# Kernel tuning notes

Measured on AMD Instinct MI355X. Metric: run time of the kernel, lower is better.

Reference implementation:

```python
import jax, jax.numpy as jnp
import numpy as np

LN_EPS = 1e-5


def layer_norm(x, g, b):
    m = jnp.mean(x, axis=-1, keepdims=True)
    v = jnp.mean((x - m) ** 2, axis=-1, keepdims=True)
    return (x - m) * jax.lax.rsqrt(v + LN_EPS) * g + b


def sppcf(x):
    # x: [B, de], de = 4*d. Multi-scale avg-pool + strided interleave assembly.
    B, de = x.shape
    d = de // 4
    p2 = x.reshape(B, de // 2, 2).mean(-1)          # kernel=2, stride=2 -> [B, 2d]
    p4 = x.reshape(B, d, 4).mean(-1)                # kernel=4, stride=4 -> [B, d]
    # kernel=16, stride=4 pooling via cumsum: out[i] = mean(x[:, 4i:4i+16]), i in [0, d-4]
    cs = jnp.concatenate([jnp.zeros((B, 1), x.dtype), jnp.cumsum(x, axis=1)], axis=1)
    starts = jnp.arange(d - 3) * 4
    p16 = (cs[:, starts + 16] - cs[:, starts]) / 16.0  # [B, d-3]
    # fused_output2[:, :-3] = p16 ; fused_output2[:, -3:] = fused_output2[:, -7:-4] = p16[:, -4:-1]
    f2 = jnp.concatenate([p16, p16[:, -4:-1]], axis=1)  # [B, d]
    # out[0::2]=p2, out[1::4]=p4, out[3::4]=f2  <=>  interleave groups of 4
    out = jnp.stack([p2[:, 0::2], p4, p2[:, 1::2], f2], axis=-1).reshape(B, de)
    return out


def setup_inputs() -> dict:
    key = jax.random.key(0)
    ks = jax.random.split(key, 8)
    B, S, C = 16384, 25, 200
    E, D, H, NC = 2, 4 * C, 32, 16  # encoder_n, dim, mlp_dim, num_classes
    inp = {
        "x": jax.random.normal(ks[0], (B, S, C), dtype=jnp.float32),
        "lnA_g": jnp.ones((E, D), jnp.float32),
        "lnA_b": jnp.zeros((E, D), jnp.float32),
        "lnB_g": jnp.ones((E, D), jnp.float32),
        "lnB_b": jnp.zeros((E, D), jnp.float32),
        "w1": jax.random.normal(ks[1], (E, D, H), jnp.float32) * (1.0 / np.sqrt(D)),
        "b1": jnp.zeros((E, H), jnp.float32),
        "w2": jax.random.normal(ks[2], (E, H, D), jnp.float32) * (1.0 / np.sqrt(H)),
        "b2": jnp.zeros((E, D), jnp.float32),
        "fc_w": jax.random.normal(ks[3], (C, NC), jnp.float32) * (1.0 / np.sqrt(C)),
        "fc_b": jnp.zeros((NC,), jnp.float32),
    }
    return inp


def reference(x, lnA_g, lnA_b, lnB_g, lnB_b, w1, b1, w2, b2, fc_w, fc_b):
    B, S, C = x.shape
    E = lnA_g.shape[0]
    # CFModule.cross_fuse: interleave min/mean/last/max over spectral-neighbor axis
    body = x[:, :-1, :]
    h = jnp.stack(
        [body.min(axis=1), body.mean(axis=1), x[:, -1, :], body.max(axis=1)], axis=-1
    ).reshape(B, 4 * C)
    for i in range(E):
        # Residual(PreNorm(SPPCFModule))
        h = h + sppcf(layer_norm(h, lnA_g[i], lnA_b[i]))
        # Residual(PreNorm(FeedForward))  (dropout=0 -> identity)
        z = layer_norm(h, lnB_g[i], lnB_b[i])
        z = jax.nn.gelu(z @ w1[i] + b1[i], approximate=False) @ w2[i] + b2[i]
        h = h + z
    # n_pool=1, channels % 1 == 0 branch: view [B, C, 4].mean then fc0
    pooled = h.reshape(B, C, 4).mean(axis=-1)
    return pooled @ fc_w + fc_b
```

## Files before the change

### kernel.cpp

```cpp
#include <hip/hip_runtime.h>
#include <math.h>

namespace {

constexpr int kC  = 200;
constexpr int kD  = 800;
constexpr int kS  = 25;
constexpr int kH  = 32;
constexpr int kNC = 16;
constexpr int kR  = 8;
constexpr int kRW = 800;

typedef float vfloat4 __attribute__((ext_vector_type(4)));

__device__ __forceinline__ int woff(int m) { return (m << 2) ^ ((m & 0x38) >> 1); }

__device__ __forceinline__ float4 ld4(const float* p) { return *(const float4*)p; }
__device__ __forceinline__ float4 ld4nt(const float* p) {
    vfloat4 v = __builtin_nontemporal_load((const vfloat4*)p);
    return make_float4(v.x, v.y, v.z, v.w);
}
__device__ __forceinline__ void   st4(float* p, float4 v) { *(float4*)p = v; }
__device__ __forceinline__ float  hsum4(float4 v) { return (v.x + v.y) + (v.z + v.w); }

__device__ __forceinline__ float4 f4fma(float s, float4 w, float4 a) {
    a.x = fmaf(s, w.x, a.x); a.y = fmaf(s, w.y, a.y);
    a.z = fmaf(s, w.z, a.z); a.w = fmaf(s, w.w, a.w);
    return a;
}

__device__ __forceinline__ void wfence() {
    asm volatile("s_waitcnt lgkmcnt(0)" ::: "memory");
}

__global__ __launch_bounds__(256)
void featurize_kernel(const float* __restrict__ x, float* __restrict__ hws, int Btot)
{
    const int gid = blockIdx.x * 256 + threadIdx.x;
    if (gid >= Btot * 50) return;
    const int row = gid / 50;
    const int cq  = gid - row * 50;

    const float* xp = x + (size_t)row * (kS * kC) + cq * 4;
    float4 v = ld4nt(xp);
    float4 mn = v, mx = v, sm = v;
    #pragma unroll
    for (int s = 1; s < kS - 1; ++s) {
        float4 u = ld4nt(xp + s * kC);
        mn.x = fminf(mn.x, u.x); mx.x = fmaxf(mx.x, u.x); sm.x += u.x;
        mn.y = fminf(mn.y, u.y); mx.y = fmaxf(mx.y, u.y); sm.y += u.y;
        mn.z = fminf(mn.z, u.z); mx.z = fmaxf(mx.z, u.z); sm.z += u.z;
        mn.w = fminf(mn.w, u.w); mx.w = fmaxf(mx.w, u.w); sm.w += u.w;
    }
    float4 last = ld4nt(xp + (kS - 1) * kC);
    const float i24 = 1.0f / 24.0f;
    float* hp = hws + (size_t)row * kD + 16 * cq;
    st4(hp + 0,  make_float4(mn.x, sm.x * i24, last.x, mx.x));
    st4(hp + 4,  make_float4(mn.y, sm.y * i24, last.y, mx.y));
    st4(hp + 8,  make_float4(mn.z, sm.z * i24, last.z, mx.z));
    st4(hp + 12, make_float4(mn.w, sm.w * i24, last.w, mx.w));
}

__device__ __forceinline__ void ln_row(const float* hrow, float* yrow,
                                       const float* __restrict__ g,
                                       const float* __restrict__ bb, int j)
{
    const bool tail = (j < 8);
    float4 v0 = ld4(&hrow[woff(j)]);
    float4 v1 = ld4(&hrow[woff(j + 64)]);
    float4 v2 = ld4(&hrow[woff(j + 128)]);
    float4 v3 = make_float4(0.f, 0.f, 0.f, 0.f);
    if (tail) v3 = ld4(&hrow[woff(192 + j)]);

    float sm = hsum4(v0) + hsum4(v1) + hsum4(v2) + hsum4(v3);
    #pragma unroll
    for (int mk = 32; mk >= 1; mk >>= 1) sm += __shfl_xor(sm, mk, 64);
    const float mean = sm * (1.0f / 800.0f);

    float ssq = 0.f;
    { float a=v0.x-mean,b=v0.y-mean,c=v0.z-mean,d=v0.w-mean; ssq += a*a+b*b+c*c+d*d; }
    { float a=v1.x-mean,b=v1.y-mean,c=v1.z-mean,d=v1.w-mean; ssq += a*a+b*b+c*c+d*d; }
    { float a=v2.x-mean,b=v2.y-mean,c=v2.z-mean,d=v2.w-mean; ssq += a*a+b*b+c*c+d*d; }
    if (tail) { float a=v3.x-mean,b=v3.y-mean,c=v3.z-mean,d=v3.w-mean; ssq += a*a+b*b+c*c+d*d; }
    #pragma unroll
    for (int mk = 32; mk >= 1; mk >>= 1) ssq += __shfl_xor(ssq, mk, 64);
    const float rstd = rsqrtf(ssq * (1.0f / 800.0f) + 1e-5f);

    auto stc = [&](int m, float4 v) {
        float4 g4 = ld4(&g[4 * m]);
        float4 b4 = ld4(&bb[4 * m]);
        float4 y;
        y.x = (v.x - mean) * rstd * g4.x + b4.x;
        y.y = (v.y - mean) * rstd * g4.y + b4.y;
        y.z = (v.z - mean) * rstd * g4.z + b4.z;
        y.w = (v.w - mean) * rstd * g4.w + b4.w;
        st4(&yrow[woff(m)], y);
    };
    stc(j, v0); stc(j + 64, v1); stc(j + 128, v2);
    if (tail) stc(192 + j, v3);
}

__device__ __forceinline__ void sppcf_add(const float* yrow, float* hrow, int j)
{
    auto one = [&](int m) {
        const int kk = (m <= 196) ? m : m - 4;
        float4 q0 = ld4(&yrow[woff(kk)]);
        float4 q1 = ld4(&yrow[woff(kk + 1)]);
        float4 q2 = ld4(&yrow[woff(kk + 2)]);
        float4 q3 = ld4(&yrow[woff(kk + 3)]);
        float4 y4 = (m <= 196) ? q0 : ld4(&yrow[woff(m)]);
        const float s16 = hsum4(q0) + hsum4(q1) + hsum4(q2) + hsum4(q3);
        float4 h4 = ld4(&hrow[woff(m)]);
        h4.x += (y4.x + y4.y) * 0.5f;
        h4.y += (y4.x + y4.y + y4.z + y4.w) * 0.25f;
        h4.z += (y4.z + y4.w) * 0.5f;
        h4.w += s16 * (1.0f / 16.0f);
        st4(&hrow[woff(m)], h4);
    };
    one(j); one(j + 64); one(j + 128);
    if (j < 8) one(192 + j);
}

template<bool FROMWS>
__global__ __launch_bounds__(256)
void essp_main(const float* __restrict__ src,
               const float* __restrict__ lnA_g, const float* __restrict__ lnA_b,
               const float* __restrict__ lnB_g, const float* __restrict__ lnB_b,
               const float* __restrict__ w1, const float* __restrict__ b1,
               const float* __restrict__ w2, const float* __restrict__ b2,
               const float* __restrict__ fc_w, const float* __restrict__ fc_b,
               float* __restrict__ out, int Btot)
{
    __shared__ float hs[kR * kRW];
    __shared__ float zb[kR * kRW];
    __shared__ float vb[kR * kH];

    const int t   = threadIdx.x;
    const int w   = t >> 6;
    const int j   = t & 63;
    const int b0  = blockIdx.x * kR;

    #pragma unroll
    for (int rr = 0; rr < 2; ++rr) {
        const int lr  = w + 4 * rr;
        const int row = b0 + lr;
        if constexpr (FROMWS) {
            if (row < Btot) {
                const float* hg = src + (size_t)row * kD;
                float* hr = &hs[lr * kRW];
                st4(&hr[woff(j)],       ld4(&hg[4 * j]));
                st4(&hr[woff(j + 64)],  ld4(&hg[4 * (j + 64)]));
                st4(&hr[woff(j + 128)], ld4(&hg[4 * (j + 128)]));
                if (j < 8) st4(&hr[woff(192 + j)], ld4(&hg[4 * (192 + j)]));
            }
        } else {
            if (j < 50 && row < Btot) {
                const float* xp = src + (size_t)row * (kS * kC) + j * 4;
                float4 v = ld4nt(xp);
                float4 mn = v, mx = v, sm = v;
                #pragma unroll
                for (int s = 1; s < kS - 1; ++s) {
                    float4 u = ld4nt(xp + s * kC);
                    mn.x = fminf(mn.x, u.x); mx.x = fmaxf(mx.x, u.x); sm.x += u.x;
                    mn.y = fminf(mn.y, u.y); mx.y = fmaxf(mx.y, u.y); sm.y += u.y;
                    mn.z = fminf(mn.z, u.z); mx.z = fmaxf(mx.z, u.z); sm.z += u.z;
                    mn.w = fminf(mn.w, u.w); mx.w = fmaxf(mx.w, u.w); sm.w += u.w;
                }
                float4 last = ld4nt(xp + (kS - 1) * kC);
                const float i24 = 1.0f / 24.0f;
                float* hr = &hs[lr * kRW];
                st4(&hr[woff(4 * j + 0)], make_float4(mn.x, sm.x * i24, last.x, mx.x));
                st4(&hr[woff(4 * j + 1)], make_float4(mn.y, sm.y * i24, last.y, mx.y));
                st4(&hr[woff(4 * j + 2)], make_float4(mn.z, sm.z * i24, last.z, mx.z));
                st4(&hr[woff(4 * j + 3)], make_float4(mn.w, sm.w * i24, last.w, mx.w));
            }
        }
    }
    wfence();

    for (int layer = 0; layer < 2; ++layer) {
        const float* gA  = lnA_g + layer * kD;
        const float* bAv = lnA_b + layer * kD;
        const float* gB  = lnB_g + layer * kD;
        const float* bBv = lnB_b + layer * kD;
        const float* w1p = w1 + layer * kD * kH;
        const float* b1p = b1 + layer * kH;
        const float* w2p = w2 + layer * kH * kD;
        const float* b2p = b2 + layer * kD;

        ln_row(&hs[w * kRW], &zb[w * kRW], gA, bAv, j);
        ln_row(&hs[(w + 4) * kRW], &zb[(w + 4) * kRW], gA, bAv, j);
        wfence();
        sppcf_add(&zb[w * kRW], &hs[w * kRW], j);
        sppcf_add(&zb[(w + 4) * kRW], &hs[(w + 4) * kRW], j);
        wfence();
        ln_row(&hs[w * kRW], &zb[w * kRW], gB, bBv, j);
        ln_row(&hs[(w + 4) * kRW], &zb[(w + 4) * kRW], gB, bBv, j);
        __syncthreads();

        float4 acc[kR];
        const int dg = t >> 3, cg = t & 7;
        #pragma unroll
        for (int r = 0; r < kR; ++r) acc[r] = make_float4(0.f, 0.f, 0.f, 0.f);
        if (t < 200) {
            #pragma unroll
            for (int cc = 0; cc < 8; ++cc) {
                const int m = dg * 8 + cc, d0 = 4 * m;
                float4 wr0 = ld4(&w1p[(d0 + 0) * kH + 4 * cg]);
                float4 wr1 = ld4(&w1p[(d0 + 1) * kH + 4 * cg]);
                float4 wr2 = ld4(&w1p[(d0 + 2) * kH + 4 * cg]);
                float4 wr3 = ld4(&w1p[(d0 + 3) * kH + 4 * cg]);
                const int wo = woff(m);
                #pragma unroll
                for (int r = 0; r < kR; ++r) {
                    float4 z = ld4(&zb[r * kRW + wo]);
                    acc[r] = f4fma(z.x, wr0, acc[r]);
                    acc[r] = f4fma(z.y, wr1, acc[r]);
                    acc[r] = f4fma(z.z, wr2, acc[r]);
                    acc[r] = f4fma(z.w, wr3, acc[r]);
                }
            }
        }
        __syncthreads();
        if (t < 200) {
            const int pb = dg * 32 + ((4 * cg) ^ ((dg & 7) << 2));
            #pragma unroll
            for (int r = 0; r < kR; ++r) st4(&zb[r * kRW + pb], acc[r]);
        }
        __syncthreads();

        {
            const int r = t >> 5, h = t & 31;
            float u = b1p[h];
            #pragma unroll
            for (int dq = 0; dq < 25; ++dq)
                u += zb[r * kRW + dq * 32 + (h ^ ((dq & 7) << 2))];
            vb[r * kH + h] = 0.5f * u * (1.0f + erff(u * 0.70710678118654752440f));
        }
        __syncthreads();

        if (t < 200) {
            float4 a2[kR];
            #pragma unroll
            for (int r = 0; r < kR; ++r) a2[r] = make_float4(0.f, 0.f, 0.f, 0.f);
            #pragma unroll
            for (int hc = 0; hc < 8; ++hc) {
                float4 wq0 = ld4(&w2p[(4*hc + 0) * kD + 4*t]);
                float4 wq1 = ld4(&w2p[(4*hc + 1) * kD + 4*t]);
                float4 wq2 = ld4(&w2p[(4*hc + 2) * kD + 4*t]);
                float4 wq3 = ld4(&w2p[(4*hc + 3) * kD + 4*t]);
                #pragma unroll
                for (int r = 0; r < kR; ++r) {
                    float4 vq = ld4(&vb[r * kH + 4*hc]);
                    a2[r] = f4fma(vq.x, wq0, a2[r]);
                    a2[r] = f4fma(vq.y, wq1, a2[r]);
                    a2[r] = f4fma(vq.z, wq2, a2[r]);
                    a2[r] = f4fma(vq.w, wq3, a2[r]);
                }
            }
            const float4 bq = ld4(&b2p[4*t]);
            const int wo = woff(t);
            #pragma unroll
            for (int r = 0; r < kR; ++r) {
                float4 h4 = ld4(&hs[r * kRW + wo]);
                h4.x += a2[r].x + bq.x; h4.y += a2[r].y + bq.y;
                h4.z += a2[r].z + bq.z; h4.w += a2[r].w + bq.w;
                st4(&hs[r * kRW + wo], h4);
            }
        }
        __syncthreads();
    }

    #pragma unroll
    for (int rr = 0; rr < 2; ++rr) {
        const int lr = w + 4 * rr;
        const float* hr = &hs[lr * kRW];
        float* pr = &zb[lr * kRW];
        pr[j]       = hsum4(ld4(&hr[woff(j)]))       * 0.25f;
        pr[j + 64]  = hsum4(ld4(&hr[woff(j + 64)]))  * 0.25f;
        pr[j + 128] = hsum4(ld4(&hr[woff(j + 128)])) * 0.25f;
        if (j < 8) pr[192 + j] = hsum4(ld4(&hr[woff(192 + j)])) * 0.25f;
    }
    wfence();

    #pragma unroll
    for (int rr = 0; rr < 2; ++rr) {
        const int lr  = w + 4 * rr;
        const int row = b0 + lr;
        const int n = j & 15, sg = j >> 4;
        const float* pr = &zb[lr * kRW + sg * 50];
        const float* fw = fc_w + (size_t)(sg * 50) * kNC + n;
        float acc = 0.f;
        #pragma unroll 10
        for (int i = 0; i < 50; ++i) acc += pr[i] * fw[i * kNC];
        acc += __shfl_xor(acc, 16, 64);
        acc += __shfl_xor(acc, 32, 64);
        if (j < kNC && row < Btot)
            out[(size_t)row * kNC + j] = acc + fc_b[j];
    }
}

}

extern "C" void kernel_launch(void* const* d_in, const int* in_sizes, int n_in,
                              void* d_out, int out_size, void* d_ws, size_t ws_size,
                              hipStream_t stream) {
    const float* x     = (const float*)d_in[0];
    const float* lnA_g = (const float*)d_in[1];
    const float* lnA_b = (const float*)d_in[2];
    const float* lnB_g = (const float*)d_in[3];
    const float* lnB_b = (const float*)d_in[4];
    const float* w1    = (const float*)d_in[5];
    const float* b1    = (const float*)d_in[6];
    const float* w2    = (const float*)d_in[7];
    const float* b2    = (const float*)d_in[8];
    const float* fc_w  = (const float*)d_in[9];
    const float* fc_b  = (const float*)d_in[10];
    float* out = (float*)d_out;

    const int Btot   = in_sizes[0] / (kS * kC);
    const int blocks = (Btot + kR - 1) / kR;
    const size_t hbytes = (size_t)Btot * kD * sizeof(float);

    if (ws_size >= hbytes) {
        float* hws = (float*)d_ws;
        const int fblocks = (Btot * 50 + 255) / 256;
        hipLaunchKernelGGL(featurize_kernel, dim3(fblocks), dim3(256), 0, stream,
                           x, hws, Btot);
        hipLaunchKernelGGL((essp_main<true>), dim3(blocks), dim3(256), 0, stream,
                           hws, lnA_g, lnA_b, lnB_g, lnB_b, w1, b1, w2, b2,
                           fc_w, fc_b, out, Btot);
    } else {
        hipLaunchKernelGGL((essp_main<false>), dim3(blocks), dim3(256), 0, stream,
                           x, lnA_g, lnA_b, lnB_g, lnB_b, w1, b1, w2, b2,
                           fc_w, fc_b, out, Btot);
    }
}
```

Baseline: 190.6 us.

## Keep residual rows in registers instead of a shared-memory buffer

Removes the per-block shared `hs` array and holds each wave's two residual rows in `float4` registers for the whole kernel. The featurized input, the SPPCF update, the FFN residual add and the final pooling all work on those registers, while `zb` is reused for normalized activations and the FFN output. This roughly halves LDS use per block, which could allow more resident blocks per CU, and it cuts LDS read/write traffic for the residual. In exchange each thread holds about 32 more live VGPRs, which may limit occupancy in a different way. Out-of-range rows are clamped to the last valid row rather than skipped.

```diff
diff --git a/kernel.cpp b/kernel.cpp
--- a/kernel.cpp
+++ b/kernel.cpp
@@ -27,6 +27,9 @@
     a.x = fmaf(s, w.x, a.x); a.y = fmaf(s, w.y, a.y);
     a.z = fmaf(s, w.z, a.z); a.w = fmaf(s, w.w, a.w);
     return a;
+}
+__device__ __forceinline__ float4 f4add(float4 a, float4 b) {
+    return make_float4(a.x + b.x, a.y + b.y, a.z + b.z, a.w + b.w);
 }
 
 __device__ __forceinline__ void wfence() {
@@ -61,27 +64,22 @@
     st4(hp + 12, make_float4(mn.w, sm.w * i24, last.w, mx.w));
 }
 
-__device__ __forceinline__ void ln_row(const float* hrow, float* yrow,
+__device__ __forceinline__ void ln_reg(float4 c0, float4 c1, float4 c2, float4 c3,
+                                       bool tail, int j,
                                        const float* __restrict__ g,
-                                       const float* __restrict__ bb, int j)
+                                       const float* __restrict__ bb,
+                                       float* yrow)
 {
-    const bool tail = (j < 8);
-    float4 v0 = ld4(&hrow[woff(j)]);
-    float4 v1 = ld4(&hrow[woff(j + 64)]);
-    float4 v2 = ld4(&hrow[woff(j + 128)]);
-    float4 v3 = make_float4(0.f, 0.f, 0.f, 0.f);
-    if (tail) v3 = ld4(&hrow[woff(192 + j)]);
-
-    float sm = hsum4(v0) + hsum4(v1) + hsum4(v2) + hsum4(v3);
+    float sm = hsum4(c0) + hsum4(c1) + hsum4(c2) + (tail ? hsum4(c3) : 0.f);
     #pragma unroll
     for (int mk = 32; mk >= 1; mk >>= 1) sm += __shfl_xor(sm, mk, 64);
     const float mean = sm * (1.0f / 800.0f);
 
     float ssq = 0.f;
-    { float a=v0.x-mean,b=v0.y-mean,c=v0.z-mean,d=v0.w-mean; ssq += a*a+b*b+c*c+d*d; }
-    { float a=v1.x-mean,b=v1.y-mean,c=v1.z-mean,d=v1.w-mean; ssq += a*a+b*b+c*c+d*d; }
-    { float a=v2.x-mean,b=v2.y-mean,c=v2.z-mean,d=v2.w-mean; ssq += a*a+b*b+c*c+d*d; }
-    if (tail) { float a=v3.x-mean,b=v3.y-mean,c=v3.z-mean,d=v3.w-mean; ssq += a*a+b*b+c*c+d*d; }
+    { float a=c0.x-mean,b=c0.y-mean,c=c0.z-mean,d=c0.w-mean; ssq += a*a+b*b+c*c+d*d; }
+    { float a=c1.x-mean,b=c1.y-mean,c=c1.z-mean,d=c1.w-mean; ssq += a*a+b*b+c*c+d*d; }
+    { float a=c2.x-mean,b=c2.y-mean,c=c2.z-mean,d=c2.w-mean; ssq += a*a+b*b+c*c+d*d; }
+    if (tail) { float a=c3.x-mean,b=c3.y-mean,c=c3.z-mean,d=c3.w-mean; ssq += a*a+b*b+c*c+d*d; }
     #pragma unroll
     for (int mk = 32; mk >= 1; mk >>= 1) ssq += __shfl_xor(ssq, mk, 64);
     const float rstd = rsqrtf(ssq * (1.0f / 800.0f) + 1e-5f);
@@ -96,29 +94,24 @@
         y.w = (v.w - mean) * rstd * g4.w + b4.w;
         st4(&yrow[woff(m)], y);
     };
-    stc(j, v0); stc(j + 64, v1); stc(j + 128, v2);
-    if (tail) stc(192 + j, v3);
-}
-
-__device__ __forceinline__ void sppcf_add(const float* yrow, float* hrow, int j)
+    stc(j, c0); stc(j + 64, c1); stc(j + 128, c2);
+    if (tail) stc(192 + j, c3);
+}
+
+__device__ __forceinline__ float4 sppcf_one(const float* yrow, int m, float4 h4)
 {
-    auto one = [&](int m) {
-        const int kk = (m <= 196) ? m : m - 4;
-        float4 q0 = ld4(&yrow[woff(kk)]);
-        float4 q1 = ld4(&yrow[woff(kk + 1)]);
-        float4 q2 = ld4(&yrow[woff(kk + 2)]);
-        float4 q3 = ld4(&yrow[woff(kk + 3)]);
-        float4 y4 = (m <= 196) ? q0 : ld4(&yrow[woff(m)]);
-        const float s16 = hsum4(q0) + hsum4(q1) + hsum4(q2) + hsum4(q3);
-        float4 h4 = ld4(&hrow[woff(m)]);
-        h4.x += (y4.x + y4.y) * 0.5f;
-        h4.y += (y4.x + y4.y + y4.z + y4.w) * 0.25f;
-        h4.z += (y4.z + y4.w) * 0.5f;
-        h4.w += s16 * (1.0f / 16.0f);
-        st4(&hrow[woff(m)], h4);
-    };
-    one(j); one(j + 64); one(j + 128);
-    if (j < 8) one(192 + j);
+    const int kk = (m <= 196) ? m : m - 4;
+    float4 q0 = ld4(&yrow[woff(kk)]);
+    float4 q1 = ld4(&yrow[woff(kk + 1)]);
+    float4 q2 = ld4(&yrow[woff(kk + 2)]);
+    float4 q3 = ld4(&yrow[woff(kk + 3)]);
+    float4 y4 = (m <= 196) ? q0 : ld4(&yrow[woff(m)]);
+    const float s16 = hsum4(q0) + hsum4(q1) + hsum4(q2) + hsum4(q3);
+    h4.x += (y4.x + y4.y) * 0.5f;
+    h4.y += (y4.x + y4.y + y4.z + y4.w) * 0.25f;
+    h4.z += (y4.z + y4.w) * 0.5f;
+    h4.w += s16 * (1.0f / 16.0f);
+    return h4;
 }
 
 template<bool FROMWS>
@@ -131,52 +124,74 @@
                const float* __restrict__ fc_w, const float* __restrict__ fc_b,
                float* __restrict__ out, int Btot)
 {
-    __shared__ float hs[kR * kRW];
     __shared__ float zb[kR * kRW];
     __shared__ float vb[kR * kH];
 
-    const int t   = threadIdx.x;
-    const int w   = t >> 6;
-    const int j   = t & 63;
-    const int b0  = blockIdx.x * kR;
-
-    #pragma unroll
-    for (int rr = 0; rr < 2; ++rr) {
-        const int lr  = w + 4 * rr;
-        const int row = b0 + lr;
+    const int t    = threadIdx.x;
+    const int w    = t >> 6;
+    const int j    = t & 63;
+    const int b0   = blockIdx.x * kR;
+    const bool tail = (j < 8);
+
+    float4 h0[4], h1[4];
+
+    {
+        const int r0 = min(b0 + w,     Btot - 1);
+        const int r1 = min(b0 + w + 4, Btot - 1);
         if constexpr (FROMWS) {
-            if (row < Btot) {
-                const float* hg = src + (size_t)row * kD;
-                float* hr = &hs[lr * kRW];
-                st4(&hr[woff(j)],       ld4(&hg[4 * j]));
-                st4(&hr[woff(j + 64)],  ld4(&hg[4 * (j + 64)]));
-                st4(&hr[woff(j + 128)], ld4(&hg[4 * (j + 128)]));
-                if (j < 8) st4(&hr[woff(192 + j)], ld4(&hg[4 * (192 + j)]));
+            const float* hg0 = src + (size_t)r0 * kD;
+            const float* hg1 = src + (size_t)r1 * kD;
+            h0[0] = ld4(&hg0[4 * j]);
+            h0[1] = ld4(&hg0[4 * (j + 64)]);
+            h0[2] = ld4(&hg0[4 * (j + 128)]);
+            h0[3] = tail ? ld4(&hg0[4 * (192 + j)]) : make_float4(0.f,0.f,0.f,0.f);
+            h1[0] = ld4(&hg1[4 * j]);
+            h1[1] = ld4(&hg1[4 * (j + 64)]);
+            h1[2] = ld4(&hg1[4 * (j + 128)]);
+            h1[3] = tail ? ld4(&hg1[4 * (192 + j)]) : make_float4(0.f,0.f,0.f,0.f);
+        } else {
+            #pragma unroll
+            for (int rr = 0; rr < 2; ++rr) {
+                const int lr  = w + 4 * rr;
+                const int row = (rr == 0) ? r0 : r1;
+                if (j < 50) {
+                    const float* xp = src + (size_t)row * (kS * kC) + j * 4;
+                    float4 v = ld4nt(xp);
+                    float4 mn = v, mx = v, sm = v;
+                    #pragma unroll
+                    for (int s = 1; s < kS - 1; ++s) {
+                        float4 u = ld4nt(xp + s * kC);
+                        mn.x = fminf(mn.x, u.x); mx.x = fmaxf(mx.x, u.x); sm.x += u.x;
+                        mn.y = fminf(mn.y, u.y); mx.y = fmaxf(mx.y, u.y); sm.y += u.y;
+                        mn.z = fminf(mn.z, u.z); mx.z = fmaxf(mx.z, u.z); sm.z += u.z;
+                        mn.w = fminf(mn.w, u.w); mx.w = fmaxf(mx.w, u.w); sm.w += u.w;
+                    }
+                    float4 last = ld4nt(xp + (kS - 1) * kC);
+                    const float i24 = 1.0f / 24.0f;
+                    float* hr = &zb[lr * kRW];
+                    st4(&hr[woff(4 * j + 0)], make_float4(mn.x, sm.x*i24, last.x, mx.x));
+                    st4(&hr[woff(4 * j + 1)], make_float4(mn.y, sm.y*i24, last.y, mx.y));
+                    st4(&hr[woff(4 * j + 2)], make_float4(mn.z, sm.z*i24, last.z, mx.z));
+                    st4(&hr[woff(4 * j + 3)], make_float4(mn.w, sm.w*i24, last.w, mx.w));
+                }
             }
-        } else {
-            if (j < 50 && row < Btot) {
-                const float* xp = src + (size_t)row * (kS * kC) + j * 4;
-                float4 v = ld4nt(xp);
-                float4 mn = v, mx = v, sm = v;
-                #pragma unroll
-                for (int s = 1; s < kS - 1; ++s) {
-                    float4 u = ld4nt(xp + s * kC);
-                    mn.x = fminf(mn.x, u.x); mx.x = fmaxf(mx.x, u.x); sm.x += u.x;
-                    mn.y = fminf(mn.y, u.y); mx.y = fmaxf(mx.y, u.y); sm.y += u.y;
-                    mn.z = fminf(mn.z, u.z); mx.z = fmaxf(mx.z, u.z); sm.z += u.z;
-                    mn.w = fminf(mn.w, u.w); mx.w = fmaxf(mx.w, u.w); sm.w += u.w;
-                }
-                float4 last = ld4nt(xp + (kS - 1) * kC);
-                const float i24 = 1.0f / 24.0f;
-                float* hr = &hs[lr * kRW];
-                st4(&hr[woff(4 * j + 0)], make_float4(mn.x, sm.x * i24, last.x, mx.x));
-                st4(&hr[woff(4 * j + 1)], make_float4(mn.y, sm.y * i24, last.y, mx.y));
-                st4(&hr[woff(4 * j + 2)], make_float4(mn.z, sm.z * i24, last.z, mx.z));
-                st4(&hr[woff(4 * j + 3)], make_float4(mn.w, sm.w * i24, last.w, mx.w));
-            }
-        }
-    }
-    wfence();
+            wfence();
+            const float* z0 = &zb[w * kRW];
+            const float* z1 = &zb[(w + 4) * kRW];
+            h0[0] = ld4(&z0[woff(j)]);
+            h0[1] = ld4(&z0[woff(j + 64)]);
+            h0[2] = ld4(&z0[woff(j + 128)]);
+            h0[3] = tail ? ld4(&z0[woff(192 + j)]) : make_float4(0.f,0.f,0.f,0.f);
+            h1[0] = ld4(&z1[woff(j)]);
+            h1[1] = ld4(&z1[woff(j + 64)]);
+            h1[2] = ld4(&z1[woff(j + 128)]);
+            h1[3] = tail ? ld4(&z1[woff(192 + j)]) : make_float4(0.f,0.f,0.f,0.f);
+            wfence();
+        }
+    }
+
+    float* yz0 = &zb[w * kRW];
+    float* yz1 = &zb[(w + 4) * kRW];
 
     for (int layer = 0; layer < 2; ++layer) {
         const float* gA  = lnA_g + layer * kD;
@@ -188,14 +203,20 @@
         const float* w2p = w2 + layer * kH * kD;
         const float* b2p = b2 + layer * kD;
 
-        ln_row(&hs[w * kRW], &zb[w * kRW], gA, bAv, j);
-        ln_row(&hs[(w + 4) * kRW], &zb[(w + 4) * kRW], gA, bAv, j);
+        ln_reg(h0[0], h0[1], h0[2], h0[3], tail, j, gA, bAv, yz0);
+        ln_reg(h1[0], h1[1], h1[2], h1[3], tail, j, gA, bAv, yz1);
         wfence();
-        sppcf_add(&zb[w * kRW], &hs[w * kRW], j);
-        sppcf_add(&zb[(w + 4) * kRW], &hs[(w + 4) * kRW], j);
+        h0[0] = sppcf_one(yz0, j, h0[0]);
+        h0[1] = sppcf_one(yz0, j + 64, h0[1]);
+        h0[2] = sppcf_one(yz0, j + 128, h0[2]);
+        if (tail) h0[3] = sppcf_one(yz0, 192 + j, h0[3]);
+        h1[0] = sppcf_one(yz1, j, h1[0]);
+        h1[1] = sppcf_one(yz1, j + 64, h1[1]);
+        h1[2] = sppcf_one(yz1, j + 128, h1[2]);
+        if (tail) h1[3] = sppcf_one(yz1, 192 + j, h1[3]);
         wfence();
-        ln_row(&hs[w * kRW], &zb[w * kRW], gB, bBv, j);
-        ln_row(&hs[(w + 4) * kRW], &zb[(w + 4) * kRW], gB, bBv, j);
+        ln_reg(h0[0], h0[1], h0[2], h0[3], tail, j, gB, bBv, yz0);
+        ln_reg(h1[0], h1[1], h1[2], h1[3], tail, j, gB, bBv, yz1);
         __syncthreads();
 
         float4 acc[kR];
@@ -251,35 +272,41 @@
                 float4 wq3 = ld4(&w2p[(4*hc + 3) * kD + 4*t]);
                 #pragma unroll
                 for (int r = 0; r < kR; ++r) {
-                    float4 vq = ld4(&vb[r * kH + 4*hc]);
+                    float4 vq = ld4(&vb[r * kH + 4 * hc]);
                     a2[r] = f4fma(vq.x, wq0, a2[r]);
                     a2[r] = f4fma(vq.y, wq1, a2[r]);
                     a2[r] = f4fma(vq.z, wq2, a2[r]);
                     a2[r] = f4fma(vq.w, wq3, a2[r]);
                 }
             }
-            const float4 bq = ld4(&b2p[4*t]);
+            const float4 bq = ld4(&b2p[4 * t]);
             const int wo = woff(t);
             #pragma unroll
-            for (int r = 0; r < kR; ++r) {
-                float4 h4 = ld4(&hs[r * kRW + wo]);
-                h4.x += a2[r].x + bq.x; h4.y += a2[r].y + bq.y;
-                h4.z += a2[r].z + bq.z; h4.w += a2[r].w + bq.w;
-                st4(&hs[r * kRW + wo], h4);
-            }
-        }
-        __syncthreads();
-    }
-
-    #pragma unroll
-    for (int rr = 0; rr < 2; ++rr) {
-        const int lr = w + 4 * rr;
-        const float* hr = &hs[lr * kRW];
-        float* pr = &zb[lr * kRW];
-        pr[j]       = hsum4(ld4(&hr[woff(j)]))       * 0.25f;
-        pr[j + 64]  = hsum4(ld4(&hr[woff(j + 64)]))  * 0.25f;
-        pr[j + 128] = hsum4(ld4(&hr[woff(j + 128)])) * 0.25f;
-        if (j < 8) pr[192 + j] = hsum4(ld4(&hr[woff(192 + j)])) * 0.25f;
+            for (int r = 0; r < kR; ++r)
+                st4(&zb[r * kRW + wo], f4add(a2[r], bq));
+        }
+        __syncthreads();
+
+        h0[0] = f4add(h0[0], ld4(&yz0[woff(j)]));
+        h0[1] = f4add(h0[1], ld4(&yz0[woff(j + 64)]));
+        h0[2] = f4add(h0[2], ld4(&yz0[woff(j + 128)]));
+        if (tail) h0[3] = f4add(h0[3], ld4(&yz0[woff(192 + j)]));
+        h1[0] = f4add(h1[0], ld4(&yz1[woff(j)]));
+        h1[1] = f4add(h1[1], ld4(&yz1[woff(j + 64)]));
+        h1[2] = f4add(h1[2], ld4(&yz1[woff(j + 128)]));
+        if (tail) h1[3] = f4add(h1[3], ld4(&yz1[woff(192 + j)]));
+        wfence();
+    }
+
+    {
+        yz0[j]       = hsum4(h0[0]) * 0.25f;
+        yz0[j + 64]  = hsum4(h0[1]) * 0.25f;
+        yz0[j + 128] = hsum4(h0[2]) * 0.25f;
+        if (tail) yz0[192 + j] = hsum4(h0[3]) * 0.25f;
+        yz1[j]       = hsum4(h1[0]) * 0.25f;
+        yz1[j + 64]  = hsum4(h1[1]) * 0.25f;
+        yz1[j + 128] = hsum4(h1[2]) * 0.25f;
+        if (tail) yz1[192 + j] = hsum4(h1[3]) * 0.25f;
     }
     wfence();
 
```

Result: slower. 257.6 us (+35.2%).

## Use 512-thread blocks with one wavefront per row in essp_main

Applied to the files above, without the earlier changes.

Doubles the block size of the main kernel to 512 threads so each of the 8 rows gets its own wavefront for the layernorm, SPPCF and final pooling stages, and the two 256-thread halves each handle 4 rows in the MLP matmuls. This halves the serial per-thread work and register accumulators (8 float4 down to 4), and launch bounds request 6 waves per SIMD to raise occupancy. The cost is that the w1/w2 weight loads are now duplicated across the two halves, and block-wide barriers must synchronise twice as many waves.

```diff
diff --git a/kernel.cpp b/kernel.cpp
--- a/kernel.cpp
+++ b/kernel.cpp
@@ -122,7 +122,7 @@
 }
 
 template<bool FROMWS>
-__global__ __launch_bounds__(256)
+__global__ __launch_bounds__(512, 6)
 void essp_main(const float* __restrict__ src,
                const float* __restrict__ lnA_g, const float* __restrict__ lnA_b,
                const float* __restrict__ lnB_g, const float* __restrict__ lnB_b,
@@ -135,45 +135,43 @@
     __shared__ float zb[kR * kRW];
     __shared__ float vb[kR * kH];
 
-    const int t   = threadIdx.x;
-    const int w   = t >> 6;
-    const int j   = t & 63;
-    const int b0  = blockIdx.x * kR;
-
-    #pragma unroll
-    for (int rr = 0; rr < 2; ++rr) {
-        const int lr  = w + 4 * rr;
-        const int row = b0 + lr;
-        if constexpr (FROMWS) {
-            if (row < Btot) {
-                const float* hg = src + (size_t)row * kD;
-                float* hr = &hs[lr * kRW];
-                st4(&hr[woff(j)],       ld4(&hg[4 * j]));
-                st4(&hr[woff(j + 64)],  ld4(&hg[4 * (j + 64)]));
-                st4(&hr[woff(j + 128)], ld4(&hg[4 * (j + 128)]));
-                if (j < 8) st4(&hr[woff(192 + j)], ld4(&hg[4 * (192 + j)]));
+    const int t    = threadIdx.x;
+    const int w    = t >> 6;
+    const int j    = t & 63;
+    const int b0   = blockIdx.x * kR;
+    const int row  = b0 + w;
+    const int base = t & 255;
+    const int half = t >> 8;
+
+    if constexpr (FROMWS) {
+        if (row < Btot) {
+            const float* hg = src + (size_t)row * kD;
+            float* hr = &hs[w * kRW];
+            st4(&hr[woff(j)],       ld4(&hg[4 * j]));
+            st4(&hr[woff(j + 64)],  ld4(&hg[4 * (j + 64)]));
+            st4(&hr[woff(j + 128)], ld4(&hg[4 * (j + 128)]));
+            if (j < 8) st4(&hr[woff(192 + j)], ld4(&hg[4 * (192 + j)]));
+        }
+    } else {
+        if (j < 50 && row < Btot) {
+            const float* xp = src + (size_t)row * (kS * kC) + j * 4;
+            float4 v = ld4nt(xp);
+            float4 mn = v, mx = v, sm = v;
+            #pragma unroll
+            for (int s = 1; s < kS - 1; ++s) {
+                float4 u = ld4nt(xp + s * kC);
+                mn.x = fminf(mn.x, u.x); mx.x = fmaxf(mx.x, u.x); sm.x += u.x;
+                mn.y = fminf(mn.y, u.y); mx.y = fmaxf(mx.y, u.y); sm.y += u.y;
+                mn.z = fminf(mn.z, u.z); mx.z = fmaxf(mx.z, u.z); sm.z += u.z;
+                mn.w = fminf(mn.w, u.w); mx.w = fmaxf(mx.w, u.w); sm.w += u.w;
             }
-        } else {
-            if (j < 50 && row < Btot) {
-                const float* xp = src + (size_t)row * (kS * kC) + j * 4;
-                float4 v = ld4nt(xp);
-                float4 mn = v, mx = v, sm = v;
-                #pragma unroll
-                for (int s = 1; s < kS - 1; ++s) {
-                    float4 u = ld4nt(xp + s * kC);
-                    mn.x = fminf(mn.x, u.x); mx.x = fmaxf(mx.x, u.x); sm.x += u.x;
-                    mn.y = fminf(mn.y, u.y); mx.y = fmaxf(mx.y, u.y); sm.y += u.y;
-                    mn.z = fminf(mn.z, u.z); mx.z = fmaxf(mx.z, u.z); sm.z += u.z;
-                    mn.w = fminf(mn.w, u.w); mx.w = fmaxf(mx.w, u.w); sm.w += u.w;
-                }
-                float4 last = ld4nt(xp + (kS - 1) * kC);
-                const float i24 = 1.0f / 24.0f;
-                float* hr = &hs[lr * kRW];
-                st4(&hr[woff(4 * j + 0)], make_float4(mn.x, sm.x * i24, last.x, mx.x));
-                st4(&hr[woff(4 * j + 1)], make_float4(mn.y, sm.y * i24, last.y, mx.y));
-                st4(&hr[woff(4 * j + 2)], make_float4(mn.z, sm.z * i24, last.z, mx.z));
-                st4(&hr[woff(4 * j + 3)], make_float4(mn.w, sm.w * i24, last.w, mx.w));
-            }
+            float4 last = ld4nt(xp + (kS - 1) * kC);
+            const float i24 = 1.0f / 24.0f;
+            float* hr = &hs[w * kRW];
+            st4(&hr[woff(4 * j + 0)], make_float4(mn.x, sm.x * i24, last.x, mx.x));
+            st4(&hr[woff(4 * j + 1)], make_float4(mn.y, sm.y * i24, last.y, mx.y));
+            st4(&hr[woff(4 * j + 2)], make_float4(mn.z, sm.z * i24, last.z, mx.z));
+            st4(&hr[woff(4 * j + 3)], make_float4(mn.w, sm.w * i24, last.w, mx.w));
         }
     }
     wfence();
@@ -189,20 +187,17 @@
         const float* b2p = b2 + layer * kD;
 
         ln_row(&hs[w * kRW], &zb[w * kRW], gA, bAv, j);
-        ln_row(&hs[(w + 4) * kRW], &zb[(w + 4) * kRW], gA, bAv, j);
         wfence();
         sppcf_add(&zb[w * kRW], &hs[w * kRW], j);
-        sppcf_add(&zb[(w + 4) * kRW], &hs[(w + 4) * kRW], j);
         wfence();
         ln_row(&hs[w * kRW], &zb[w * kRW], gB, bBv, j);
-        ln_row(&hs[(w + 4) * kRW], &zb[(w + 4) * kRW], gB, bBv, j);
-        __syncthreads();
-
-        float4 acc[kR];
-        const int dg = t >> 3, cg = t & 7;
+        __syncthreads();
+
+        float4 acc[4];
+        const int dg = base >> 3, cg = base & 7;
         #pragma unroll
-        for (int r = 0; r < kR; ++r) acc[r] = make_float4(0.f, 0.f, 0.f, 0.f);
-        if (t < 200) {
+        for (int r = 0; r < 4; ++r) acc[r] = make_float4(0.f, 0.f, 0.f, 0.f);
+        if (base < 200) {
             #pragma unroll
             for (int cc = 0; cc < 8; ++cc) {
                 const int m = dg * 8 + cc, d0 = 4 * m;
@@ -212,8 +207,8 @@
                 float4 wr3 = ld4(&w1p[(d0 + 3) * kH + 4 * cg]);
                 const int wo = woff(m);
                 #pragma unroll
-                for (int r = 0; r < kR; ++r) {
-                    float4 z = ld4(&zb[r * kRW + wo]);
+                for (int r = 0; r < 4; ++r) {
+                    float4 z = ld4(&zb[(4 * half + r) * kRW + wo]);
                     acc[r] = f4fma(z.x, wr0, acc[r]);
                     acc[r] = f4fma(z.y, wr1, acc[r]);
                     acc[r] = f4fma(z.z, wr2, acc[r]);
@@ -222,14 +217,15 @@
             }
         }
         __syncthreads();
-        if (t < 200) {
+        if (base < 200) {
             const int pb = dg * 32 + ((4 * cg) ^ ((dg & 7) << 2));
             #pragma unroll
-            for (int r = 0; r < kR; ++r) st4(&zb[r * kRW + pb], acc[r]);
-        }
-        __syncthreads();
-
-        {
+            for (int r = 0; r < 4; ++r)
+                st4(&zb[(4 * half + r) * kRW + pb], acc[r]);
+        }
+        __syncthreads();
+
+        if (t < 256) {
             const int r = t >> 5, h = t & 31;
             float u = b1p[h];
             #pragma unroll
@@ -239,43 +235,42 @@
         }
         __syncthreads();
 
-        if (t < 200) {
-            float4 a2[kR];
-            #pragma unroll
-            for (int r = 0; r < kR; ++r) a2[r] = make_float4(0.f, 0.f, 0.f, 0.f);
+        if (base < 200) {
+            float4 a2[4];
+            #pragma unroll
+            for (int r = 0; r < 4; ++r) a2[r] = make_float4(0.f, 0.f, 0.f, 0.f);
             #pragma unroll
             for (int hc = 0; hc < 8; ++hc) {
-                float4 wq0 = ld4(&w2p[(4*hc + 0) * kD + 4*t]);
-                float4 wq1 = ld4(&w2p[(4*hc + 1) * kD + 4*t]);
-                float4 wq2 = ld4(&w2p[(4*hc + 2) * kD + 4*t]);
-                float4 wq3 = ld4(&w2p[(4*hc + 3) * kD + 4*t]);
+                float4 wq0 = ld4(&w2p[(4*hc + 0) * kD + 4*base]);
+                float4 wq1 = ld4(&w2p[(4*hc + 1) * kD + 4*base]);
+                float4 wq2 = ld4(&w2p[(4*hc + 2) * kD + 4*base]);
+                float4 wq3 = ld4(&w2p[(4*hc + 3) * kD + 4*base]);
                 #pragma unroll
-                for (int r = 0; r < kR; ++r) {
-                    float4 vq = ld4(&vb[r * kH + 4*hc]);
+                for (int r = 0; r < 4; ++r) {
+                    float4 vq = ld4(&vb[(4 * half + r) * kH + 4 * hc]);
                     a2[r] = f4fma(vq.x, wq0, a2[r]);
                     a2[r] = f4fma(vq.y, wq1, a2[r]);
                     a2[r] = f4fma(vq.z, wq2, a2[r]);
                     a2[r] = f4fma(vq.w, wq3, a2[r]);
                 }
             }
-            const float4 bq = ld4(&b2p[4*t]);
-            const int wo = woff(t);
-            #pragma unroll
-            for (int r = 0; r < kR; ++r) {
-                float4 h4 = ld4(&hs[r * kRW + wo]);
+            const float4 bq = ld4(&b2p[4 * base]);
+            const int wo = woff(base);
+            #pragma unroll
+            for (int r = 0; r < 4; ++r) {
+                float* hp = &hs[(4 * half + r) * kRW + wo];
+                float4 h4 = ld4(hp);
                 h4.x += a2[r].x + bq.x; h4.y += a2[r].y + bq.y;
                 h4.z += a2[r].z + bq.z; h4.w += a2[r].w + bq.w;
-                st4(&hs[r * kRW + wo], h4);
+                st4(hp, h4);
             }
         }
         __syncthreads();
     }
 
-    #pragma unroll
-    for (int rr = 0; rr < 2; ++rr) {
-        const int lr = w + 4 * rr;
-        const float* hr = &hs[lr * kRW];
-        float* pr = &zb[lr * kRW];
+    {
+        const float* hr = &hs[w * kRW];
+        float* pr = &zb[w * kRW];
         pr[j]       = hsum4(ld4(&hr[woff(j)]))       * 0.25f;
         pr[j + 64]  = hsum4(ld4(&hr[woff(j + 64)]))  * 0.25f;
         pr[j + 128] = hsum4(ld4(&hr[woff(j + 128)])) * 0.25f;
@@ -283,12 +278,9 @@
     }
     wfence();
 
-    #pragma unroll
-    for (int rr = 0; rr < 2; ++rr) {
-        const int lr  = w + 4 * rr;
-        const int row = b0 + lr;
+    {
         const int n = j & 15, sg = j >> 4;
-        const float* pr = &zb[lr * kRW + sg * 50];
+        const float* pr = &zb[w * kRW + sg * 50];
         const float* fw = fc_w + (size_t)(sg * 50) * kNC + n;
         float acc = 0.f;
         #pragma unroll 10
@@ -327,11 +319,11 @@
         const int fblocks = (Btot * 50 + 255) / 256;
         hipLaunchKernelGGL(featurize_kernel, dim3(fblocks), dim3(256), 0, stream,
                            x, hws, Btot);
-        hipLaunchKernelGGL((essp_main<true>), dim3(blocks), dim3(256), 0, stream,
+        hipLaunchKernelGGL((essp_main<true>), dim3(blocks), dim3(512), 0, stream,
                            hws, lnA_g, lnA_b, lnB_g, lnB_b, w1, b1, w2, b2,
                            fc_w, fc_b, out, Btot);
     } else {
-        hipLaunchKernelGGL((essp_main<false>), dim3(blocks), dim3(256), 0, stream,
+        hipLaunchKernelGGL((essp_main<false>), dim3(blocks), dim3(512), 0, stream,
                            x, lnA_g, lnA_b, lnB_g, lnB_b, w1, b1, w2, b2,
                            fc_w, fc_b, out, Btot);
     }
```

Measured after the change: 274.4 us. 44.0% more time.

## Make FFN per-wavefront to drop block barriers and cross-thread reduction buffer

Applied to the files above, without the earlier changes.

Restructures both MLP matmuls so each wavefront handles only its own two rows. The first matmul splits K across 4 lane groups reduced by xor-shuffles, and the second covers 200 column chunks across lanes. This removes the block-wide __syncthreads and the shared-memory partial-sum pass, replacing them with wave-local lgkmcnt fences. In exchange each weight element is now loaded from global/L1 by every wavefront rather than reused across 8 rows in registers, which raises weight traffic per block.

```diff
diff --git a/kernel.cpp b/kernel.cpp
--- a/kernel.cpp
+++ b/kernel.cpp
@@ -27,6 +27,20 @@
     a.x = fmaf(s, w.x, a.x); a.y = fmaf(s, w.y, a.y);
     a.z = fmaf(s, w.z, a.z); a.w = fmaf(s, w.w, a.w);
     return a;
+}
+__device__ __forceinline__ float4 f4add(float4 a, float4 b) {
+    return make_float4(a.x + b.x, a.y + b.y, a.z + b.z, a.w + b.w);
+}
+__device__ __forceinline__ float4 shfl4_xor(float4 v, int m) {
+    return make_float4(__shfl_xor(v.x, m, 64), __shfl_xor(v.y, m, 64),
+                       __shfl_xor(v.z, m, 64), __shfl_xor(v.w, m, 64));
+}
+__device__ __forceinline__ float4 gelu4(float4 u) {
+    const float k = 0.70710678118654752440f;
+    return make_float4(0.5f * u.x * (1.0f + erff(u.x * k)),
+                       0.5f * u.y * (1.0f + erff(u.y * k)),
+                       0.5f * u.z * (1.0f + erff(u.z * k)),
+                       0.5f * u.w * (1.0f + erff(u.w * k)));
 }
 
 __device__ __forceinline__ void wfence() {
@@ -139,6 +153,12 @@
     const int w   = t >> 6;
     const int j   = t & 63;
     const int b0  = blockIdx.x * kR;
+    const int lr0 = w, lr1 = w + 4;
+
+    const int r_    = j >> 5;
+    const int kseg  = (j >> 3) & 3;
+    const int hq    = j & 7;
+    const int lrm   = w + 4 * r_;
 
     #pragma unroll
     for (int rr = 0; rr < 2; ++rr) {
@@ -188,87 +208,77 @@
         const float* w2p = w2 + layer * kH * kD;
         const float* b2p = b2 + layer * kD;
 
-        ln_row(&hs[w * kRW], &zb[w * kRW], gA, bAv, j);
-        ln_row(&hs[(w + 4) * kRW], &zb[(w + 4) * kRW], gA, bAv, j);
-        wfence();
-        sppcf_add(&zb[w * kRW], &hs[w * kRW], j);
-        sppcf_add(&zb[(w + 4) * kRW], &hs[(w + 4) * kRW], j);
-        wfence();
-        ln_row(&hs[w * kRW], &zb[w * kRW], gB, bBv, j);
-        ln_row(&hs[(w + 4) * kRW], &zb[(w + 4) * kRW], gB, bBv, j);
-        __syncthreads();
-
-        float4 acc[kR];
-        const int dg = t >> 3, cg = t & 7;
-        #pragma unroll
-        for (int r = 0; r < kR; ++r) acc[r] = make_float4(0.f, 0.f, 0.f, 0.f);
-        if (t < 200) {
-            #pragma unroll
-            for (int cc = 0; cc < 8; ++cc) {
-                const int m = dg * 8 + cc, d0 = 4 * m;
-                float4 wr0 = ld4(&w1p[(d0 + 0) * kH + 4 * cg]);
-                float4 wr1 = ld4(&w1p[(d0 + 1) * kH + 4 * cg]);
-                float4 wr2 = ld4(&w1p[(d0 + 2) * kH + 4 * cg]);
-                float4 wr3 = ld4(&w1p[(d0 + 3) * kH + 4 * cg]);
+        ln_row(&hs[lr0 * kRW], &zb[lr0 * kRW], gA, bAv, j);
+        ln_row(&hs[lr1 * kRW], &zb[lr1 * kRW], gA, bAv, j);
+        wfence();
+        sppcf_add(&zb[lr0 * kRW], &hs[lr0 * kRW], j);
+        sppcf_add(&zb[lr1 * kRW], &hs[lr1 * kRW], j);
+        wfence();
+        ln_row(&hs[lr0 * kRW], &zb[lr0 * kRW], gB, bBv, j);
+        ln_row(&hs[lr1 * kRW], &zb[lr1 * kRW], gB, bBv, j);
+        wfence();
+
+        {
+            const float* zrow = &zb[lrm * kRW];
+            float4 uacc = make_float4(0.f, 0.f, 0.f, 0.f);
+            #pragma unroll 5
+            for (int c = 0; c < 50; ++c) {
+                const int m = kseg * 50 + c;
+                float4 z4 = ld4(&zrow[woff(m)]);
+                float4 w0 = ld4(&w1p[(4 * m + 0) * kH + 4 * hq]);
+                float4 w1q = ld4(&w1p[(4 * m + 1) * kH + 4 * hq]);
+                float4 w2q = ld4(&w1p[(4 * m + 2) * kH + 4 * hq]);
+                float4 w3q = ld4(&w1p[(4 * m + 3) * kH + 4 * hq]);
+                uacc = f4fma(z4.x, w0,  uacc);
+                uacc = f4fma(z4.y, w1q, uacc);
+                uacc = f4fma(z4.z, w2q, uacc);
+                uacc = f4fma(z4.w, w3q, uacc);
+            }
+            uacc = f4add(uacc, shfl4_xor(uacc, 8));
+            uacc = f4add(uacc, shfl4_xor(uacc, 16));
+            float4 b1q = ld4(&b1p[4 * hq]);
+            float4 v4  = gelu4(f4add(uacc, b1q));
+            if (kseg == 0) st4(&vb[lrm * kH + 4 * hq], v4);
+        }
+        wfence();
+
+        {
+            auto mm2_chunk = [&](int m) {
+                float4 a0 = make_float4(0.f, 0.f, 0.f, 0.f), a1 = a0;
+                #pragma unroll
+                for (int hc = 0; hc < 8; ++hc) {
+                    float4 wq0 = ld4(&w2p[(4 * hc + 0) * kD + 4 * m]);
+                    float4 wq1 = ld4(&w2p[(4 * hc + 1) * kD + 4 * m]);
+                    float4 wq2 = ld4(&w2p[(4 * hc + 2) * kD + 4 * m]);
+                    float4 wq3 = ld4(&w2p[(4 * hc + 3) * kD + 4 * m]);
+                    float4 v0 = ld4(&vb[lr0 * kH + 4 * hc]);
+                    a0 = f4fma(v0.x, wq0, a0); a0 = f4fma(v0.y, wq1, a0);
+                    a0 = f4fma(v0.z, wq2, a0); a0 = f4fma(v0.w, wq3, a0);
+                    float4 v1 = ld4(&vb[lr1 * kH + 4 * hc]);
+                    a1 = f4fma(v1.x, wq0, a1); a1 = f4fma(v1.y, wq1, a1);
+                    a1 = f4fma(v1.z, wq2, a1); a1 = f4fma(v1.w, wq3, a1);
+                }
+                float4 bq = ld4(&b2p[4 * m]);
                 const int wo = woff(m);
-                #pragma unroll
-                for (int r = 0; r < kR; ++r) {
-                    float4 z = ld4(&zb[r * kRW + wo]);
-                    acc[r] = f4fma(z.x, wr0, acc[r]);
-                    acc[r] = f4fma(z.y, wr1, acc[r]);
-                    acc[r] = f4fma(z.z, wr2, acc[r]);
-                    acc[r] = f4fma(z.w, wr3, acc[r]);
+                {
+                    float4 h4 = ld4(&hs[lr0 * kRW + wo]);
+                    h4.x += a0.x + bq.x; h4.y += a0.y + bq.y;
+                    h4.z += a0.z + bq.z; h4.w += a0.w + bq.w;
+                    st4(&hs[lr0 * kRW + wo], h4);
                 }
-            }
+                {
+                    float4 h4 = ld4(&hs[lr1 * kRW + wo]);
+                    h4.x += a1.x + bq.x; h4.y += a1.y + bq.y;
+                    h4.z += a1.z + bq.z; h4.w += a1.w + bq.w;
+                    st4(&hs[lr1 * kRW + wo], h4);
+                }
+            };
+            mm2_chunk(j);
+            mm2_chunk(j + 64);
+            mm2_chunk(j + 128);
+            if (j < 8) mm2_chunk(192 + j);
         }
-        __syncthreads();
-        if (t < 200) {
-            const int pb = dg * 32 + ((4 * cg) ^ ((dg & 7) << 2));
-            #pragma unroll
-            for (int r = 0; r < kR; ++r) st4(&zb[r * kRW + pb], acc[r]);
-        }
-        __syncthreads();
-
-        {
-            const int r = t >> 5, h = t & 31;
-            float u = b1p[h];
-            #pragma unroll
-            for (int dq = 0; dq < 25; ++dq)
-                u += zb[r * kRW + dq * 32 + (h ^ ((dq & 7) << 2))];
-            vb[r * kH + h] = 0.5f * u * (1.0f + erff(u * 0.70710678118654752440f));
-        }
-        __syncthreads();
-
-        if (t < 200) {
-            float4 a2[kR];
-            #pragma unroll
-            for (int r = 0; r < kR; ++r) a2[r] = make_float4(0.f, 0.f, 0.f, 0.f);
-            #pragma unroll
-            for (int hc = 0; hc < 8; ++hc) {
-                float4 wq0 = ld4(&w2p[(4*hc + 0) * kD + 4*t]);
-                float4 wq1 = ld4(&w2p[(4*hc + 1) * kD + 4*t]);
-                float4 wq2 = ld4(&w2p[(4*hc + 2) * kD + 4*t]);
-                float4 wq3 = ld4(&w2p[(4*hc + 3) * kD + 4*t]);
-                #pragma unroll
-                for (int r = 0; r < kR; ++r) {
-                    float4 vq = ld4(&vb[r * kH + 4*hc]);
-                    a2[r] = f4fma(vq.x, wq0, a2[r]);
-                    a2[r] = f4fma(vq.y, wq1, a2[r]);
-                    a2[r] = f4fma(vq.z, wq2, a2[r]);
-                    a2[r] = f4fma(vq.w, wq3, a2[r]);
-                }
-            }
-            const float4 bq = ld4(&b2p[4*t]);
-            const int wo = woff(t);
-            #pragma unroll
-            for (int r = 0; r < kR; ++r) {
-                float4 h4 = ld4(&hs[r * kRW + wo]);
-                h4.x += a2[r].x + bq.x; h4.y += a2[r].y + bq.y;
-                h4.z += a2[r].z + bq.z; h4.w += a2[r].w + bq.w;
-                st4(&hs[r * kRW + wo], h4);
-            }
-        }
-        __syncthreads();
+        wfence();
     }
 
     #pragma unroll
```

Result: slower. 395.0 us (+107.2%).
